# Performance work log

Measured on AMD Instinct MI355X. Metric: run time of the kernel, lower is better.

The kernel has to match this reference:

```python
import jax, jax.numpy as jnp
import numpy as np

OT_REG = 0.1
OT_ITERS = 10
LN_EPS = 1e-5


def layernorm(x, g, b):
    m = jnp.mean(x, axis=-1, keepdims=True)
    v = jnp.mean((x - m) ** 2, axis=-1, keepdims=True)
    return (x - m) * jax.lax.rsqrt(v + LN_EPS) * g + b


def sinkhorn(C, epsilon, iters):
    # standard Sinkhorn: kernel exp(C/eps), alternate row/col normalization
    Q = jnp.exp(C / epsilon)  # [Na,B,La,Lb]
    def body(_, Q):
        Q = Q / jnp.sum(Q, axis=-1, keepdims=True)
        Q = Q / jnp.sum(Q, axis=-2, keepdims=True)
        return Q
    return jax.lax.fori_loop(0, iters, body, Q)


def setup_inputs() -> dict:
    key = jax.random.key(0)
    ks = jax.random.split(key, 16)
    Na, La, B, Lb, Din, H = 32, 32, 64, 32, 768, 768
    s = 0.02
    return {
        "entity_cls": jax.random.normal(ks[0], (Na, Din), jnp.float32),
        "entity_tokens": jax.random.normal(ks[1], (Na, La, Din), jnp.float32),
        "mention_cls": jax.random.normal(ks[2], (B, Din), jnp.float32),
        "mention_tokens": jax.random.normal(ks[3], (B, Lb, Din), jnp.float32),
        "Wq": jax.random.normal(ks[4], (Din, H), jnp.float32) * s,
        "bq": jnp.zeros((H,), jnp.float32),
        "Wk": jax.random.normal(ks[5], (Din, H), jnp.float32) * s,
        "bk": jnp.zeros((H,), jnp.float32),
        "Wv": jax.random.normal(ks[6], (Din, H), jnp.float32) * s,
        "bv": jnp.zeros((H,), jnp.float32),
        "ln1_g": jnp.ones((H,), jnp.float32),
        "ln1_b": jnp.zeros((H,), jnp.float32),
        "Wcls": jax.random.normal(ks[7], (Din, H), jnp.float32) * s,
        "bcls": jnp.zeros((H,), jnp.float32),
        "Wsp": jax.random.normal(ks[8], (H, 1), jnp.float32) * s,
        "bsp": jnp.zeros((1,), jnp.float32),
        "ln2_g": jnp.ones((H,), jnp.float32),
        "ln2_b": jnp.zeros((H,), jnp.float32),
    }


def reference(entity_cls, entity_tokens, mention_cls, mention_tokens,
              Wq, bq, Wk, bk, Wv, bv, ln1_g, ln1_b,
              Wcls, bcls, Wsp, bsp, ln2_g, ln2_b):
    # projections
    q = entity_tokens @ Wq + bq      # [Na,La,H]
    k = mention_tokens @ Wk + bk     # [B,Lb,H]
    v = mention_tokens @ Wv + bv     # [B,Lb,H]

    # cross-batch cosine similarity: [Na,B,La,Lb]
    qn = q / jnp.maximum(jnp.linalg.norm(q, axis=-1, keepdims=True), 1e-8)
    kn = k / jnp.maximum(jnp.linalg.norm(k, axis=-1, keepdims=True), 1e-8)
    C = jnp.einsum('aid,bjd->abij', qn, kn)

    # Sinkhorn on detached cost (torch uses C.detach())
    T = sinkhorn(jax.lax.stop_gradient(C), OT_REG, OT_ITERS)
    # F.normalize(dim=-1): L2 normalize last dim
    T = T / jnp.maximum(jnp.linalg.norm(T, axis=-1, keepdims=True), 1e-12)

    # attention + residual + layernorm: [Na,B,La,H]
    attended = jnp.einsum('abij,bjd->abid', T, v) + q[:, None, :, :]
    attended = layernorm(attended, ln1_g, ln1_b)

    # softpool over token dim (-2)
    w = jax.nn.softmax(attended @ Wsp + bsp, axis=-2)   # [Na,B,La,1]
    pooled = jnp.sum(attended * w, axis=-2)             # [Na,B,H]
    context = layernorm(pooled, ln2_g, ln2_b)

    # matching scores
    ecls = entity_cls @ Wcls + bcls                     # [Na,H]
    g2l = jnp.sum(ecls[:, None, :] * context, axis=-1)  # [Na,B]
    g2l = g2l.T                                         # [B,Na]
    g2g = mention_cls @ entity_cls.T                    # [B,Na]
    return (g2l + g2g) * 0.5
```

## Files before the change

### kernel.cpp

```cpp
#include <hip/hip_runtime.h>
#include <math.h>


typedef __attribute__((ext_vector_type(8))) short bfrag8;
typedef __attribute__((ext_vector_type(4))) float f32x4;

__device__ __forceinline__ unsigned short f2bf(float x) {
  union { float f; unsigned u; } v; v.f = x;
  unsigned r = v.u + 0x7fffu + ((v.u >> 16) & 1u);
  return (unsigned short)(r >> 16);
}

template <int CTRL>
__device__ __forceinline__ float dpp_add(float x) {
  union { float f; int i; } a, b;
  a.f = x;
  b.i = __builtin_amdgcn_update_dpp(0, a.i, CTRL, 0xf, 0xf, true);
  return x + b.f;
}
__device__ __forceinline__ float sum16(float x) {
  x = dpp_add<0xB1>(x);
  x = dpp_add<0x4E>(x);
  x = dpp_add<0x124>(x);
  x = dpp_add<0x128>(x);
  return x;
}

__global__ __launch_bounds__(256) void prep_kernel(
    const float* __restrict__ a0, const float* __restrict__ a1, const float* __restrict__ a2,
    unsigned short* __restrict__ o0, unsigned short* __restrict__ o1, unsigned short* __restrict__ o2,
    float* __restrict__ nrm,
    const float* __restrict__ W0, const float* __restrict__ W1,
    const float* __restrict__ W2, const float* __restrict__ W3,
    unsigned short* __restrict__ T0, unsigned short* __restrict__ T1,
    unsigned short* __restrict__ T2, unsigned short* __restrict__ T3) {
  __shared__ float t[32][33];
  int bx = blockIdx.x;
  if (bx < 2331) {
    if (bx < 2328) {
      const float* in; unsigned short* out; int i, n4;
      if (bx < 768)       { in = a0; out = o0; i = bx * 256 + threadIdx.x;          n4 = 196608; }
      else if (bx < 2304) { in = a1; out = o1; i = (bx - 768) * 256 + threadIdx.x;  n4 = 393216; }
      else                { in = a2; out = o2; i = (bx - 2304) * 256 + threadIdx.x; n4 = 6144; }
      if (i >= n4) return;
      float4 f = ((const float4*)in)[i];
      ushort4 o;
      o.x = f2bf(f.x); o.y = f2bf(f.y); o.z = f2bf(f.z); o.w = f2bf(f.w);
      ((ushort4*)out)[i] = o;
    } else {
      int i = (bx - 2328) * 256 + threadIdx.x;
      if (i < 768) ((float4*)nrm)[i] = make_float4(0.f, 0.f, 0.f, 0.f);
    }
    return;
  }
  int idx = bx - 2331;
  int z = idx / 576, r2 = idx % 576;
  int tby = r2 / 24, tbx = r2 % 24;
  const float* W = (z == 0) ? W0 : (z == 1) ? W1 : (z == 2) ? W2 : W3;
  unsigned short* O = (z == 0) ? T0 : (z == 1) ? T1 : (z == 2) ? T2 : T3;
  const int gx = tbx * 32, gy = tby * 32;
  const int tx = threadIdx.x & 31, ty = threadIdx.x >> 5;
#pragma unroll
  for (int u = 0; u < 4; ++u) {
    int row = ty + u * 8;
    t[row][tx] = W[(size_t)(gy + row) * 768 + gx + tx];
  }
  __syncthreads();
#pragma unroll
  for (int u = 0; u < 4; ++u) {
    int row = ty + u * 8;
    O[(size_t)(gx + row) * 768 + gy + tx] = f2bf(t[tx][row]);
  }
}

__global__ __launch_bounds__(512, 2) void proj_gemm_kernel(
    const unsigned short* __restrict__ Ae, const unsigned short* __restrict__ Am,
    const unsigned short* __restrict__ Acls,
    const unsigned short* __restrict__ WqT, const unsigned short* __restrict__ WkT,
    const unsigned short* __restrict__ WvT, const unsigned short* __restrict__ WclsT,
    const float* __restrict__ bq, const float* __restrict__ bk,
    const float* __restrict__ bv, const float* __restrict__ bcls,
    unsigned short* __restrict__ qb, unsigned short* __restrict__ qT,
    unsigned short* __restrict__ kb, unsigned short* __restrict__ vT,
    float* __restrict__ ecls, float* __restrict__ iq_sq, float* __restrict__ ik_sq) {
  const int z = blockIdx.z;
  const int M = (z == 0) ? 1024 : (z == 3) ? 32 : 2048;
  const int bm = blockIdx.y * 128;
  if (bm >= M) return;
  const unsigned short* A = (z == 3) ? Acls : (z == 0) ? Ae : Am;
  const unsigned short* B = (z == 0) ? WqT : (z == 1) ? WkT : (z == 2) ? WvT : WclsT;
  const float* bias = (z == 0) ? bq : (z == 1) ? bk : (z == 2) ? bv : bcls;

  __shared__ unsigned short As[128 * 64];
  __shared__ unsigned short Bs[128 * 64];
  const int t = threadIdx.x;
  const int bn = blockIdx.x * 128;
  const int l = t & 63, w = t >> 6;
  const int wm = w & 3, wn = w >> 2;
  const int cg = l & 15, rq = l >> 4;

  f32x4 acc[2][4];
#pragma unroll
  for (int mi = 0; mi < 2; ++mi)
#pragma unroll
    for (int nj = 0; nj < 4; ++nj) { f32x4 zz = {0.f, 0.f, 0.f, 0.f}; acc[mi][nj] = zz; }

  for (int k0 = 0; k0 < 768; k0 += 64) {
    __syncthreads();
#pragma unroll
    for (int u = 0; u < 2; ++u) {
      int c = t + u * 512;
      int row = c >> 3, kc = c & 7;
      int gm = bm + row; gm = gm < M ? gm : M - 1;
      int4 av = *(const int4*)(A + (size_t)gm * 768 + k0 + kc * 8);
      *(int4*)(As + row * 64 + ((kc ^ (row & 7)) * 8)) = av;
      int4 bv4 = *(const int4*)(B + (size_t)(bn + row) * 768 + k0 + kc * 8);
      *(int4*)(Bs + row * 64 + ((kc ^ (row & 7)) * 8)) = bv4;
    }
    __syncthreads();
#pragma unroll
    for (int kk = 0; kk < 2; ++kk) {
      bfrag8 af[2], bf[4];
      const int kc = kk * 4 + rq;
#pragma unroll
      for (int mi = 0; mi < 2; ++mi) {
        int arow = wm * 32 + mi * 16 + cg;
        af[mi] = *(const bfrag8*)(As + arow * 64 + ((kc ^ (arow & 7)) * 8));
      }
#pragma unroll
      for (int nj = 0; nj < 4; ++nj) {
        int brow = wn * 64 + nj * 16 + cg;
        bf[nj] = *(const bfrag8*)(Bs + brow * 64 + ((kc ^ (brow & 7)) * 8));
      }
#pragma unroll
      for (int mi = 0; mi < 2; ++mi)
#pragma unroll
        for (int nj = 0; nj < 4; ++nj)
          acc[mi][nj] = __builtin_amdgcn_mfma_f32_16x16x32_bf16(af[mi], bf[nj], acc[mi][nj], 0, 0, 0);
    }
  }

  float p[2][4] = {};
#pragma unroll
  for (int mi = 0; mi < 2; ++mi) {
#pragma unroll
    for (int nj = 0; nj < 4; ++nj) {
      int gn = bn + wn * 64 + nj * 16 + cg;
      float bs = bias[gn];
#pragma unroll
      for (int r = 0; r < 4; ++r) {
        int gm = bm + wm * 32 + mi * 16 + rq * 4 + r;
        if (gm >= M) continue;
        float val = acc[mi][nj][r] + bs;
        if (z < 2) p[mi][r] += val * val;
        unsigned short bfv = f2bf(val);
        if (z == 0) {
          qb[(size_t)gm * 768 + gn] = bfv;
          int at = gm >> 5, j = gm & 31;
          qT[((size_t)at * 768 + gn) * 32 + j] = bfv;
        } else if (z == 1) kb[(size_t)gm * 768 + gn] = bfv;
        else if (z == 2) {
          int bb = gm >> 5, j = gm & 31;
          vT[((size_t)bb * 768 + gn) * 32 + j] = bfv;
        } else ecls[(size_t)gm * 768 + gn] = val;
      }
    }
  }
  if (z < 2) {
    float* nrm = (z == 0) ? iq_sq : ik_sq;
#pragma unroll
    for (int mi = 0; mi < 2; ++mi)
#pragma unroll
      for (int r = 0; r < 4; ++r) {
        float s = sum16(p[mi][r]);
        if (cg == 0) {
          int gm = bm + wm * 32 + mi * 16 + rq * 4 + r;
          atomicAdd(&nrm[gm], s);
        }
      }
  }
}

__global__ __launch_bounds__(1024, 1) void cos_attn_kernel(
    const unsigned short* __restrict__ qb, const unsigned short* __restrict__ kb,
    const float* __restrict__ iq_sq, const float* __restrict__ ik_sq,
    const unsigned short* __restrict__ qT,
    const unsigned short* __restrict__ vT,
    const float* __restrict__ ln1_g, const float* __restrict__ ln1_b,
    const float* __restrict__ Wsp, const float* __restrict__ bsp,
    const float* __restrict__ ln2_g, const float* __restrict__ ln2_b,
    const float* __restrict__ ecls,
    const float* __restrict__ entity_cls, const float* __restrict__ mention_cls,
    float* __restrict__ out) {
  __shared__ unsigned short vLds[2 * 768 * 32];
  __shared__ __align__(16) unsigned short scratch[12288];
  __shared__ float gabLds[4 * 768];
  __shared__ float gwLds[768];
  __shared__ float ldsIq[128], ldsIk[64];
  __shared__ float red[160];
  __shared__ float xch[1584];

  unsigned short* As = scratch;
  unsigned short* Bs = scratch + 8192;
  unsigned short* Tlds = scratch;

  const int t = threadIdx.x;
  const int l = t & 63, w = t >> 6;
  const int p = w >> 1, q = w & 1;
  const int bm = blockIdx.y * 128, bn = blockIdx.x * 64;
  const int wm = p & 3, wn = p >> 2;
  const int cg = l & 15, rq = l >> 4;

  {
    float sgw = 0.f, sbw = 0.f, sga[4] = {}, sba[4] = {};
    for (int h = t; h < 768; h += 1024) {
      float g1 = ln1_g[h], b1 = ln1_b[h], wsp = Wsp[h];
      float g2 = ln2_g[h], b2 = ln2_b[h];
      float gw = g1 * wsp;
      gwLds[h] = gw;
      sgw += gw; sbw += b1 * wsp;
#pragma unroll
      for (int aa = 0; aa < 4; ++aa) {
        float ec = ecls[(size_t)((blockIdx.y << 2) + aa) * 768 + h];
        float gab = g2 * ec;
        gabLds[aa * 768 + h] = gab;
        sga[aa] += gab; sba[aa] += b2 * ec;
      }
    }
    sgw = sum16(sgw); sbw = sum16(sbw);
#pragma unroll
    for (int aa = 0; aa < 4; ++aa) { sga[aa] = sum16(sga[aa]); sba[aa] = sum16(sba[aa]); }
#pragma unroll
    for (int m = 16; m < 64; m <<= 1) {
      sgw += __shfl_xor(sgw, m); sbw += __shfl_xor(sbw, m);
#pragma unroll
      for (int aa = 0; aa < 4; ++aa) { sga[aa] += __shfl_xor(sga[aa], m); sba[aa] += __shfl_xor(sba[aa], m); }
    }
    if (l == 0) {
      red[w * 10 + 0] = sgw; red[w * 10 + 1] = sbw;
#pragma unroll
      for (int aa = 0; aa < 4; ++aa) { red[w * 10 + 2 + aa] = sga[aa]; red[w * 10 + 6 + aa] = sba[aa]; }
    }
  }
  if (t < 128) ldsIq[t] = iq_sq[bm + t];
  else if (t < 192) ldsIk[t - 128] = ik_sq[bn + t - 128];

  const int4* vsrc = (const int4*)(vT + (size_t)(blockIdx.x * 2) * 768 * 32);
  int4* vdst = (int4*)vLds;

  f32x4 acc[2];
#pragma unroll
  for (int nj = 0; nj < 2; ++nj) { f32x4 zz = {0.f, 0.f, 0.f, 0.f}; acc[nj] = zz; }

  for (int k0 = 0, s = 0; k0 < 768; k0 += 64, ++s) {
    __syncthreads();
    {
      int row = t >> 3, kc = t & 7;
      int4 av = *(const int4*)(qb + (size_t)(bm + row) * 768 + k0 + kc * 8);
      *(int4*)(As + row * 64 + ((kc ^ (row & 7)) * 8)) = av;
    }
    if (t < 512) {
      int row = t >> 3, kc = t & 7;
      int4 bv4 = *(const int4*)(kb + (size_t)(bn + row) * 768 + k0 + kc * 8);
      *(int4*)(Bs + row * 64 + ((kc ^ (row & 7)) * 8)) = bv4;
    } else {
      int tt = t - 512;
      vdst[tt + s * 512] = vsrc[tt + s * 512];
    }
    __syncthreads();
#pragma unroll
    for (int kk = 0; kk < 2; ++kk) {
      const int kc = kk * 4 + rq;
      const int arow = wm * 32 + q * 16 + cg;
      bfrag8 af = *(const bfrag8*)(As + arow * 64 + ((kc ^ (arow & 7)) * 8));
      bfrag8 bf[2];
#pragma unroll
      for (int nj = 0; nj < 2; ++nj) {
        int brow = wn * 32 + nj * 16 + cg;
        bf[nj] = *(const bfrag8*)(Bs + brow * 64 + ((kc ^ (brow & 7)) * 8));
      }
#pragma unroll
      for (int nj = 0; nj < 2; ++nj)
        acc[nj] = __builtin_amdgcn_mfma_f32_16x16x32_bf16(af, bf[nj], acc[nj], 0, 0, 0);
    }
  }

  float irow[4], icol[2];
#pragma unroll
  for (int r = 0; r < 4; ++r) {
    float sv = ldsIq[wm * 32 + q * 16 + rq * 4 + r];
    irow[r] = 1.0f / fmaxf(sqrtf(sv), 1e-8f);
  }
#pragma unroll
  for (int nj = 0; nj < 2; ++nj) {
    float sv = ldsIk[wn * 32 + nj * 16 + cg];
    icol[nj] = 1.0f / fmaxf(sqrtf(sv), 1e-8f);
  }
#pragma unroll
  for (int nj = 0; nj < 2; ++nj)
#pragma unroll
    for (int r = 0; r < 4; ++r)
      acc[nj][r] = __expf(acc[nj][r] * irow[r] * icol[nj] * 10.0f);

  for (int it = 0; it < 10; ++it) {
#pragma unroll
    for (int r = 0; r < 4; ++r) {
      float rs = sum16(acc[0][r] + acc[1][r]);
      float rinv = __builtin_amdgcn_rcpf(rs);
      acc[0][r] *= rinv; acc[1][r] *= rinv;
    }
    float colp[2];
#pragma unroll
    for (int nj = 0; nj < 2; ++nj) {
      float cl = acc[nj][0] + acc[nj][1] + acc[nj][2] + acc[nj][3];
      cl += __shfl_xor(cl, 16); cl += __shfl_xor(cl, 32);
      colp[nj] = cl;
      if (rq == 0) xch[(it & 1) * 512 + w * 32 + nj * 16 + cg] = cl;
    }
    __syncthreads();
#pragma unroll
    for (int nj = 0; nj < 2; ++nj) {
      float cs = colp[nj] + xch[(it & 1) * 512 + (w ^ 1) * 32 + nj * 16 + cg];
      float cinv = __builtin_amdgcn_rcpf(cs);
#pragma unroll
      for (int r = 0; r < 4; ++r) acc[nj][r] *= cinv;
    }
  }

#pragma unroll
  for (int r = 0; r < 4; ++r) {
    float ss = sum16(acc[0][r] * acc[0][r] + acc[1][r] * acc[1][r]);
    float tinv = 1.0f / fmaxf(sqrtf(ss), 1e-12f);
    acc[0][r] *= tinv; acc[1][r] *= tinv;
  }

  __syncthreads();
  {
    unsigned short* base = Tlds + (p << 10);
#pragma unroll
    for (int nj = 0; nj < 2; ++nj)
#pragma unroll
      for (int r = 0; r < 4; ++r)
        base[(q * 16 + rq * 4 + r) * 32 + nj * 16 + cg] = f2bf(acc[nj][r]);
  }
  __syncthreads();

  const int bl = p >> 2, ah = p & 3;
  const int b_g = (blockIdx.x << 1) + bl;
  const int a_g = (blockIdx.y << 2) + ah;
  const unsigned short* vbase = vLds + bl * 24576;

  float sgw_f = 0.f, sbw_f = 0.f, sga_f = 0.f, sba_f = 0.f;
#pragma unroll
  for (int wv = 0; wv < 16; ++wv) {
    sgw_f += red[wv * 10 + 0]; sbw_f += red[wv * 10 + 1];
    sga_f += red[wv * 10 + 2 + ah]; sba_f += red[wv * 10 + 6 + ah];
  }
  sbw_f += bsp[0];

  const unsigned short* qTa = qT + (size_t)a_g * 24576;
  const unsigned short* Tp = Tlds + (p << 10);
  bfrag8 af[2], afI[2];
#pragma unroll
  for (int mi = 0; mi < 2; ++mi) {
    af[mi] = *(const bfrag8*)(Tp + (mi * 16 + cg) * 32 + rq * 8);
    int row = mi * 16 + cg;
    bfrag8 fI;
#pragma unroll
    for (int u = 0; u < 8; ++u) fI[u] = (row == rq * 8 + u) ? (short)0x3F80 : (short)0;
    afI[mi] = fI;
  }

  float s1[2][4] = {}, s2[2][4] = {}, a1[2][4] = {};
#pragma unroll 4
  for (int j = 0; j < 24; ++j) {
    int nj = q * 24 + j;
    int h = nj * 16 + cg;
    bfrag8 vf = *(const bfrag8*)(vbase + h * 32 + rq * 8);
    bfrag8 qf = *(const bfrag8*)(qTa + (size_t)h * 32 + rq * 8);
    float gw = gwLds[h];
#pragma unroll
    for (int mi = 0; mi < 2; ++mi) {
      f32x4 zz = {0.f, 0.f, 0.f, 0.f};
      f32x4 pr = __builtin_amdgcn_mfma_f32_16x16x32_bf16(af[mi], vf, zz, 0, 0, 0);
      f32x4 x4 = __builtin_amdgcn_mfma_f32_16x16x32_bf16(afI[mi], qf, pr, 0, 0, 0);
#pragma unroll
      for (int r = 0; r < 4; ++r) {
        float x = x4[r];
        s1[mi][r] += x; s2[mi][r] += x * x; a1[mi][r] += x * gw;
      }
    }
  }
#pragma unroll
  for (int mi = 0; mi < 2; ++mi)
#pragma unroll
    for (int r = 0; r < 4; ++r) {
      s1[mi][r] = sum16(s1[mi][r]);
      s2[mi][r] = sum16(s2[mi][r]);
      a1[mi][r] = sum16(a1[mi][r]);
    }
  if (cg == 0) {
#pragma unroll
    for (int mi = 0; mi < 2; ++mi)
#pragma unroll
      for (int r = 0; r < 4; ++r) {
        int row = mi * 16 + rq * 4 + r;
        xch[(w * 3 + 0) * 32 + row] = s1[mi][r];
        xch[(w * 3 + 1) * 32 + row] = s2[mi][r];
        xch[(w * 3 + 2) * 32 + row] = a1[mi][r];
      }
  }
  __syncthreads();
  {
    const int pw = w ^ 1;
#pragma unroll
    for (int mi = 0; mi < 2; ++mi)
#pragma unroll
      for (int r = 0; r < 4; ++r) {
        int row = mi * 16 + rq * 4 + r;
        s1[mi][r] += xch[(pw * 3 + 0) * 32 + row];
        s2[mi][r] += xch[(pw * 3 + 1) * 32 + row];
        a1[mi][r] += xch[(pw * 3 + 2) * 32 + row];
      }
  }

  float uu[2][4], c0;
  {
    float mean[2][4], rstd[2][4], logit[2][4];
#pragma unroll
    for (int mi = 0; mi < 2; ++mi)
#pragma unroll
      for (int r = 0; r < 4; ++r) {
        float m1 = s1[mi][r] * (1.0f / 768.0f);
        float var = s2[mi][r] * (1.0f / 768.0f) - m1 * m1;
        float rs = rsqrtf(var + 1e-5f);
        mean[mi][r] = m1; rstd[mi][r] = rs;
        logit[mi][r] = rs * (a1[mi][r] - m1 * sgw_f) + sbw_f;
      }
    float mx = logit[0][0];
#pragma unroll
    for (int mi = 0; mi < 2; ++mi)
#pragma unroll
      for (int r = 0; r < 4; ++r) mx = fmaxf(mx, logit[mi][r]);
    mx = fmaxf(mx, __shfl_xor(mx, 16)); mx = fmaxf(mx, __shfl_xor(mx, 32));
    float se = 0.f, ee[2][4];
#pragma unroll
    for (int mi = 0; mi < 2; ++mi)
#pragma unroll
      for (int r = 0; r < 4; ++r) { ee[mi][r] = __expf(logit[mi][r] - mx); se += ee[mi][r]; }
    se += __shfl_xor(se, 16); se += __shfl_xor(se, 32);
    const float sinv = __builtin_amdgcn_rcpf(se);
    float c0a = 0.f;
#pragma unroll
    for (int mi = 0; mi < 2; ++mi)
#pragma unroll
      for (int r = 0; r < 4; ++r) {
        uu[mi][r] = ee[mi][r] * sinv * rstd[mi][r];
        c0a += uu[mi][r] * mean[mi][r];
      }
    c0a += __shfl_xor(c0a, 16); c0a += __shfl_xor(c0a, 32);
    c0 = c0a;
  }

  float ps = 0.f, pq = 0.f, spc = 0.f;
#pragma unroll 4
  for (int j = 0; j < 24; ++j) {
    int nj = q * 24 + j;
    int h = nj * 16 + cg;
    bfrag8 vf = *(const bfrag8*)(vbase + h * 32 + rq * 8);
    bfrag8 qf = *(const bfrag8*)(qTa + (size_t)h * 32 + rq * 8);
    float pp = 0.f;
#pragma unroll
    for (int mi = 0; mi < 2; ++mi) {
      f32x4 zz = {0.f, 0.f, 0.f, 0.f};
      f32x4 pr = __builtin_amdgcn_mfma_f32_16x16x32_bf16(af[mi], vf, zz, 0, 0, 0);
      f32x4 x4 = __builtin_amdgcn_mfma_f32_16x16x32_bf16(afI[mi], qf, pr, 0, 0, 0);
#pragma unroll
      for (int r = 0; r < 4; ++r) pp += uu[mi][r] * x4[r];
    }
    pp += __shfl_xor(pp, 16); pp += __shfl_xor(pp, 32);
    float pooled = ln1_g[h] * (pp - c0) + ln1_b[h];
    ps += pooled; pq += pooled * pooled;
    spc += pooled * gabLds[ah * 768 + h];
  }
  ps = sum16(ps); pq = sum16(pq); spc = sum16(spc);
  if (l == 0) {
    xch[1536 + w * 3 + 0] = ps;
    xch[1536 + w * 3 + 1] = pq;
    xch[1536 + w * 3 + 2] = spc;
  }
  __syncthreads();
  {
    const int pw = w ^ 1;
    ps += xch[1536 + pw * 3 + 0];
    pq += xch[1536 + pw * 3 + 1];
    spc += xch[1536 + pw * 3 + 2];
  }
  const float m2 = ps * (1.0f / 768.0f);
  const float var2 = pq * (1.0f / 768.0f) - m2 * m2;
  const float rs2 = rsqrtf(var2 + 1e-5f);
  const float* ea = entity_cls + (size_t)a_g * 768;
  const float* mb = mention_cls + (size_t)b_g * 768;
  float sg = 0.f;
#pragma unroll
  for (int u = 0; u < 12; ++u) sg += mb[l * 12 + u] * ea[l * 12 + u];
  sg = sum16(sg);
  sg += __shfl_xor(sg, 16); sg += __shfl_xor(sg, 32);
  float tot = rs2 * (spc - m2 * sga_f) + sba_f + sg;
  if (l == 0 && q == 0) out[b_g * 32 + a_g] = 0.5f * tot;
}

extern "C" void kernel_launch(void* const* d_in, const int* in_sizes, int n_in,
                              void* d_out, int out_size, void* d_ws, size_t ws_size,
                              hipStream_t stream) {
  const float* entity_cls     = (const float*)d_in[0];
  const float* entity_tokens  = (const float*)d_in[1];
  const float* mention_cls    = (const float*)d_in[2];
  const float* mention_tokens = (const float*)d_in[3];
  const float* Wq = (const float*)d_in[4];   const float* bq = (const float*)d_in[5];
  const float* Wk = (const float*)d_in[6];   const float* bk = (const float*)d_in[7];
  const float* Wv = (const float*)d_in[8];   const float* bv = (const float*)d_in[9];
  const float* ln1_g = (const float*)d_in[10]; const float* ln1_b = (const float*)d_in[11];
  const float* Wcls = (const float*)d_in[12];  const float* bcls = (const float*)d_in[13];
  const float* Wsp = (const float*)d_in[14];   const float* bsp = (const float*)d_in[15];
  const float* ln2_g = (const float*)d_in[16]; const float* ln2_b = (const float*)d_in[17];
  float* out = (float*)d_out;

  float* ws     = (float*)d_ws;
  float* ecls   = ws;
  float* iq_sq  = ecls + 24576;
  float* ik_sq  = iq_sq + 1024;
  unsigned short* qb = (unsigned short*)(ws + 55168);
  unsigned short* qT = qb + 786432;
  unsigned short* kb = qT + 786432;
  unsigned short* vT = kb + 1572864;
  char* R = (char*)(vT + 1572864);
  unsigned short* Ae    = (unsigned short*)R;
  unsigned short* Am    = Ae + 786432;
  unsigned short* Acls  = Am + 1572864;
  unsigned short* WqT   = Acls + 24576;
  unsigned short* WkT   = WqT + 589824;
  unsigned short* WvT   = WkT + 589824;
  unsigned short* WclsT = WvT + 589824;

  prep_kernel<<<dim3(4635), dim3(256), 0, stream>>>(
      entity_tokens, mention_tokens, entity_cls, Ae, Am, Acls, iq_sq,
      Wq, Wk, Wv, Wcls, WqT, WkT, WvT, WclsT);
  proj_gemm_kernel<<<dim3(6, 16, 4), dim3(512), 0, stream>>>(
      Ae, Am, Acls, WqT, WkT, WvT, WclsT, bq, bk, bv, bcls,
      qb, qT, kb, vT, ecls, iq_sq, ik_sq);
  cos_attn_kernel<<<dim3(32, 8), dim3(1024), 0, stream>>>(
      qb, kb, iq_sq, ik_sq, qT, vT,
      ln1_g, ln1_b, Wsp, bsp, ln2_g, ln2_b,
      ecls, entity_cls, mention_cls, out);
}
```

Before: 188.9 us.

## Split cos_attn blocks to one mention per block with 512 threads

Reworks the fused cosine/Sinkhorn/attention kernel so each block handles one mention batch (32 columns) and four entities with 512 threads instead of two mentions with 1024 threads. The grid doubles to 64x8 and launch bounds allow two blocks per CU, and shared memory shrinks by dropping the second V slab and the gab table, which is now computed from ln2_g and ecls read from global memory. This aims for better occupancy and latency hiding, at the cost of loading the 128-row Q tile twice as often and doing extra global reads in the pooling loop.

```diff
diff --git a/kernel.cpp b/kernel.cpp
--- a/kernel.cpp
+++ b/kernel.cpp
@@ -181,7 +181,7 @@
   }
 }
 
-__global__ __launch_bounds__(1024, 1) void cos_attn_kernel(
+__global__ __launch_bounds__(512, 2) void cos_attn_kernel(
     const unsigned short* __restrict__ qb, const unsigned short* __restrict__ kb,
     const float* __restrict__ iq_sq, const float* __restrict__ ik_sq,
     const unsigned short* __restrict__ qT,
@@ -192,13 +192,12 @@
     const float* __restrict__ ecls,
     const float* __restrict__ entity_cls, const float* __restrict__ mention_cls,
     float* __restrict__ out) {
-  __shared__ unsigned short vLds[2 * 768 * 32];
-  __shared__ __align__(16) unsigned short scratch[12288];
-  __shared__ float gabLds[4 * 768];
+  __shared__ unsigned short vLds[768 * 32];
+  __shared__ __align__(16) unsigned short scratch[10240];
   __shared__ float gwLds[768];
-  __shared__ float ldsIq[128], ldsIk[64];
-  __shared__ float red[160];
-  __shared__ float xch[1584];
+  __shared__ float ldsIq[128], ldsIk[32];
+  __shared__ float red[80];
+  __shared__ float xch[792];
 
   unsigned short* As = scratch;
   unsigned short* Bs = scratch + 8192;
@@ -207,13 +206,13 @@
   const int t = threadIdx.x;
   const int l = t & 63, w = t >> 6;
   const int p = w >> 1, q = w & 1;
-  const int bm = blockIdx.y * 128, bn = blockIdx.x * 64;
-  const int wm = p & 3, wn = p >> 2;
+  const int bm = blockIdx.y * 128;
+  const int b_g = blockIdx.x;
   const int cg = l & 15, rq = l >> 4;
 
   {
     float sgw = 0.f, sbw = 0.f, sga[4] = {}, sba[4] = {};
-    for (int h = t; h < 768; h += 1024) {
+    for (int h = t; h < 768; h += 512) {
       float g1 = ln1_g[h], b1 = ln1_b[h], wsp = Wsp[h];
       float g2 = ln2_g[h], b2 = ln2_b[h];
       float gw = g1 * wsp;
@@ -222,9 +221,7 @@
 #pragma unroll
       for (int aa = 0; aa < 4; ++aa) {
         float ec = ecls[(size_t)((blockIdx.y << 2) + aa) * 768 + h];
-        float gab = g2 * ec;
-        gabLds[aa * 768 + h] = gab;
-        sga[aa] += gab; sba[aa] += b2 * ec;
+        sga[aa] += g2 * ec; sba[aa] += b2 * ec;
       }
     }
     sgw = sum16(sgw); sbw = sum16(sbw);
@@ -243,9 +240,9 @@
     }
   }
   if (t < 128) ldsIq[t] = iq_sq[bm + t];
-  else if (t < 192) ldsIk[t - 128] = ik_sq[bn + t - 128];
-
-  const int4* vsrc = (const int4*)(vT + (size_t)(blockIdx.x * 2) * 768 * 32);
+  else if (t < 160) ldsIk[t - 128] = ik_sq[b_g * 32 + (t - 128)];
+
+  const int4* vsrc = (const int4*)(vT + (size_t)b_g * 768 * 32);
   int4* vdst = (int4*)vLds;
 
   f32x4 acc[2];
@@ -254,29 +251,31 @@
 
   for (int k0 = 0, s = 0; k0 < 768; k0 += 64, ++s) {
     __syncthreads();
-    {
-      int row = t >> 3, kc = t & 7;
+#pragma unroll
+    for (int u = 0; u < 2; ++u) {
+      int c = t + u * 512;
+      int row = c >> 3, kc = c & 7;
       int4 av = *(const int4*)(qb + (size_t)(bm + row) * 768 + k0 + kc * 8);
       *(int4*)(As + row * 64 + ((kc ^ (row & 7)) * 8)) = av;
     }
-    if (t < 512) {
+    if (t < 256) {
       int row = t >> 3, kc = t & 7;
-      int4 bv4 = *(const int4*)(kb + (size_t)(bn + row) * 768 + k0 + kc * 8);
+      int4 bv4 = *(const int4*)(kb + (size_t)(b_g * 32 + row) * 768 + k0 + kc * 8);
       *(int4*)(Bs + row * 64 + ((kc ^ (row & 7)) * 8)) = bv4;
     } else {
-      int tt = t - 512;
-      vdst[tt + s * 512] = vsrc[tt + s * 512];
+      int tt = t - 256;
+      vdst[tt + s * 256] = vsrc[tt + s * 256];
     }
     __syncthreads();
 #pragma unroll
     for (int kk = 0; kk < 2; ++kk) {
       const int kc = kk * 4 + rq;
-      const int arow = wm * 32 + q * 16 + cg;
+      const int arow = p * 32 + q * 16 + cg;
       bfrag8 af = *(const bfrag8*)(As + arow * 64 + ((kc ^ (arow & 7)) * 8));
       bfrag8 bf[2];
 #pragma unroll
       for (int nj = 0; nj < 2; ++nj) {
-        int brow = wn * 32 + nj * 16 + cg;
+        int brow = nj * 16 + cg;
         bf[nj] = *(const bfrag8*)(Bs + brow * 64 + ((kc ^ (brow & 7)) * 8));
       }
 #pragma unroll
@@ -288,12 +287,12 @@
   float irow[4], icol[2];
 #pragma unroll
   for (int r = 0; r < 4; ++r) {
-    float sv = ldsIq[wm * 32 + q * 16 + rq * 4 + r];
+    float sv = ldsIq[p * 32 + q * 16 + rq * 4 + r];
     irow[r] = 1.0f / fmaxf(sqrtf(sv), 1e-8f);
   }
 #pragma unroll
   for (int nj = 0; nj < 2; ++nj) {
-    float sv = ldsIk[wn * 32 + nj * 16 + cg];
+    float sv = ldsIk[nj * 16 + cg];
     icol[nj] = 1.0f / fmaxf(sqrtf(sv), 1e-8f);
   }
 #pragma unroll
@@ -315,12 +314,12 @@
       float cl = acc[nj][0] + acc[nj][1] + acc[nj][2] + acc[nj][3];
       cl += __shfl_xor(cl, 16); cl += __shfl_xor(cl, 32);
       colp[nj] = cl;
-      if (rq == 0) xch[(it & 1) * 512 + w * 32 + nj * 16 + cg] = cl;
+      if (rq == 0) xch[(it & 1) * 256 + w * 32 + nj * 16 + cg] = cl;
     }
     __syncthreads();
 #pragma unroll
     for (int nj = 0; nj < 2; ++nj) {
-      float cs = colp[nj] + xch[(it & 1) * 512 + (w ^ 1) * 32 + nj * 16 + cg];
+      float cs = colp[nj] + xch[(it & 1) * 256 + (w ^ 1) * 32 + nj * 16 + cg];
       float cinv = __builtin_amdgcn_rcpf(cs);
 #pragma unroll
       for (int r = 0; r < 4; ++r) acc[nj][r] *= cinv;
@@ -345,20 +344,18 @@
   }
   __syncthreads();
 
-  const int bl = p >> 2, ah = p & 3;
-  const int b_g = (blockIdx.x << 1) + bl;
-  const int a_g = (blockIdx.y << 2) + ah;
-  const unsigned short* vbase = vLds + bl * 24576;
+  const int a_g = (blockIdx.y << 2) + p;
 
   float sgw_f = 0.f, sbw_f = 0.f, sga_f = 0.f, sba_f = 0.f;
 #pragma unroll
-  for (int wv = 0; wv < 16; ++wv) {
+  for (int wv = 0; wv < 8; ++wv) {
     sgw_f += red[wv * 10 + 0]; sbw_f += red[wv * 10 + 1];
-    sga_f += red[wv * 10 + 2 + ah]; sba_f += red[wv * 10 + 6 + ah];
+    sga_f += red[wv * 10 + 2 + p]; sba_f += red[wv * 10 + 6 + p];
   }
   sbw_f += bsp[0];
 
   const unsigned short* qTa = qT + (size_t)a_g * 24576;
+  const float* gabg = ecls + (size_t)a_g * 768;
   const unsigned short* Tp = Tlds + (p << 10);
   bfrag8 af[2], afI[2];
 #pragma unroll
@@ -376,7 +373,7 @@
   for (int j = 0; j < 24; ++j) {
     int nj = q * 24 + j;
     int h = nj * 16 + cg;
-    bfrag8 vf = *(const bfrag8*)(vbase + h * 32 + rq * 8);
+    bfrag8 vf = *(const bfrag8*)(vLds + h * 32 + rq * 8);
     bfrag8 qf = *(const bfrag8*)(qTa + (size_t)h * 32 + rq * 8);
     float gw = gwLds[h];
 #pragma unroll
@@ -467,7 +464,7 @@
   for (int j = 0; j < 24; ++j) {
     int nj = q * 24 + j;
     int h = nj * 16 + cg;
-    bfrag8 vf = *(const bfrag8*)(vbase + h * 32 + rq * 8);
+    bfrag8 vf = *(const bfrag8*)(vLds + h * 32 + rq * 8);
     bfrag8 qf = *(const bfrag8*)(qTa + (size_t)h * 32 + rq * 8);
     float pp = 0.f;
 #pragma unroll
@@ -481,20 +478,20 @@
     pp += __shfl_xor(pp, 16); pp += __shfl_xor(pp, 32);
     float pooled = ln1_g[h] * (pp - c0) + ln1_b[h];
     ps += pooled; pq += pooled * pooled;
-    spc += pooled * gabLds[ah * 768 + h];
+    spc += pooled * (ln2_g[h] * gabg[h]);
   }
   ps = sum16(ps); pq = sum16(pq); spc = sum16(spc);
   if (l == 0) {
-    xch[1536 + w * 3 + 0] = ps;
-    xch[1536 + w * 3 + 1] = pq;
-    xch[1536 + w * 3 + 2] = spc;
+    xch[768 + w * 3 + 0] = ps;
+    xch[768 + w * 3 + 1] = pq;
+    xch[768 + w * 3 + 2] = spc;
   }
   __syncthreads();
   {
     const int pw = w ^ 1;
-    ps += xch[1536 + pw * 3 + 0];
-    pq += xch[1536 + pw * 3 + 1];
-    spc += xch[1536 + pw * 3 + 2];
+    ps += xch[768 + pw * 3 + 0];
+    pq += xch[768 + pw * 3 + 1];
+    spc += xch[768 + pw * 3 + 2];
   }
   const float m2 = ps * (1.0f / 768.0f);
   const float var2 = pq * (1.0f / 768.0f) - m2 * m2;
@@ -549,7 +546,7 @@
   proj_gemm_kernel<<<dim3(6, 16, 4), dim3(512), 0, stream>>>(
       Ae, Am, Acls, WqT, WkT, WvT, WclsT, bq, bk, bv, bcls,
       qb, qT, kb, vT, ecls, iq_sq, ik_sq);
-  cos_attn_kernel<<<dim3(32, 8), dim3(1024), 0, stream>>>(
+  cos_attn_kernel<<<dim3(64, 8), dim3(512), 0, stream>>>(
       qb, kb, iq_sq, ik_sq, qT, vT,
       ln1_g, ln1_b, Wsp, bsp, ln2_g, ln2_b,
       ecls, entity_cls, mention_cls, out);
```

New measurement: 174.3 us. -7.8%, faster.
